# Kernel optimization log

Hardware: AMD Instinct MI355X
Metric: run time of the kernel (lower is better)

The kernel has to match this reference:

```python
import jax, jax.numpy as jnp
import numpy as np
from functools import partial

N, F_IN, P, OUT, E = 100000, 8, 12, 32, 3200000


def setup_inputs() -> dict:
    key = jax.random.key(0)
    ks = jax.random.split(key, 20)
    x = jax.random.normal(ks[0], (N, F_IN, P), dtype=jnp.float32)
    edge_index = jax.random.randint(ks[1], (2, E), 0, N, dtype=jnp.int64)
    edge_weight = jax.random.uniform(ks[2], (E,), dtype=jnp.float32)
    s = 1.0 / np.sqrt(F_IN)
    s2 = 1.0 / np.sqrt(2 * OUT)
    u = lambda k, sh, sc: jax.random.uniform(k, sh, jnp.float32, -sc, sc)
    params = dict(
        Wz=u(ks[3], (F_IN, OUT), s), bz=u(ks[4], (OUT,), s),
        Wr=u(ks[5], (F_IN, OUT), s), br=u(ks[6], (OUT,), s),
        Wh=u(ks[7], (F_IN, OUT), s), bh=u(ks[8], (OUT,), s),
        Lz=u(ks[9], (2 * OUT, OUT), s2), lbz=u(ks[10], (OUT,), s2),
        Lr=u(ks[11], (2 * OUT, OUT), s2), lbr=u(ks[12], (OUT,), s2),
        Lh=u(ks[13], (2 * OUT, OUT), s2), lbh=u(ks[14], (OUT,), s2),
        att=jax.random.uniform(ks[15], (P,), jnp.float32),
        Wp=u(ks[16], (OUT, 1), 1.0 / np.sqrt(OUT)), bp=u(ks[17], (1,), 1.0 / np.sqrt(OUT)),
    )
    return {"x": x, "edge_index": edge_index, "edge_weight": edge_weight, **params}


def reference(x, edge_index, edge_weight, Wz, bz, Wr, br, Wh, bh,
              Lz, lbz, Lr, lbr, Lh, lbh, att, Wp, bp):
    n = x.shape[0]
    # GCN normalization with self-loops: D^-1/2 (A + I) D^-1/2
    loop = jnp.arange(n)
    src = jnp.concatenate([edge_index[0], loop])
    dst = jnp.concatenate([edge_index[1], loop])
    w = jnp.concatenate([edge_weight, jnp.ones((n,), edge_weight.dtype)])
    deg = jax.ops.segment_sum(w, dst, num_segments=n)
    dinv = jnp.where(deg > 0, jax.lax.rsqrt(jnp.maximum(deg, 1e-30)), 0.0)
    norm = dinv[src] * w * dinv[dst]  # [E+N]

    def prop(X):  # gather-scale-scatter aggregation, X: [N, OUT]
        return jax.ops.segment_sum(X[src] * norm[:, None], dst, num_segments=n)

    def cell(H, Xt):  # TGCN GRU cell, Xt: [N, F_IN]
        cz = prop(Xt @ Wz) + bz
        cr = prop(Xt @ Wr) + br
        ch = prop(Xt @ Wh) + bh
        Z = jax.nn.sigmoid(jnp.concatenate([cz, H], axis=1) @ Lz + lbz)
        R = jax.nn.sigmoid(jnp.concatenate([cr, H], axis=1) @ Lr + lbr)
        Ht = jnp.tanh(jnp.concatenate([ch, R * H], axis=1) @ Lh + lbh)
        return Z * H + (1.0 - Z) * Ht

    probs = jax.nn.softmax(att)
    Xts = jnp.moveaxis(x, -1, 0)  # [P, N, F_IN]

    def scan_fn(carry, inp):
        H, acc = carry
        Xt, p = inp
        Hn = cell(H, Xt)
        return (Hn, acc + p * Hn), None

    H0 = jnp.zeros((n, OUT), x.dtype)
    (_, Hacc), _ = jax.lax.scan(scan_fn, (H0, H0), (Xts, probs))

    h = jax.nn.relu(Hacc)  # dropout is identity in eval mode
    delta = h @ Wp + bp  # [N, 1]
    out = jax.nn.relu(delta + x[:, 1, -1:])
    return out
```

## Files before the change

### kernel.cpp

```cpp
#include <hip/hip_runtime.h>
#include <cstddef>

typedef __attribute__((ext_vector_type(8))) short bf16x8;
typedef __attribute__((ext_vector_type(4))) float f32x4;

#define MFMA_B16(a, b, c) __builtin_amdgcn_mfma_f32_16x16x32_bf16(a, b, c, 0, 0, 0)

#define DEV_INLINE __device__ __forceinline__

#define NPB 128
#define NPB_SHIFT 7
#define NOCT 8
#define OCT_SHIFT 14

#define QSCALE (127.0f / 6.0f)
#define QDEC   (6.0f / 127.0f)

DEV_INLINE float rcp_fast(float x) { return __builtin_amdgcn_rcpf(x); }
DEV_INLINE float sigf(float x) { return rcp_fast(1.0f + __expf(-x)); }
DEV_INLINE float tanh_fast(float x) { return 1.0f - 2.0f * rcp_fast(__expf(2.0f * x) + 1.0f); }

DEV_INLINE unsigned short f2bf(float f) {
    union { float f; unsigned u; } v; v.f = f;
    unsigned r = v.u + 0x7fffu + ((v.u >> 16) & 1u);
    return (unsigned short)(r >> 16);
}

DEV_INLINE unsigned cvt_pk_bf16(float lo, float hi) {
    unsigned r;
    asm("v_cvt_pk_bf16_f32 %0, %1, %2" : "=v"(r) : "v"(lo), "v"(hi));
    return r;
}
DEV_INLINE float bf2f(unsigned short h) {
    union { unsigned u; float f; } t; t.u = ((unsigned)h) << 16; return t.f;
}

__global__ __launch_bounds__(256) void k_cast(const float* __restrict__ x,
                                              signed char* __restrict__ Xb8, int n) {
    __shared__ float s[64 * 97];
    const int tid = threadIdx.x;
    const int nbase = blockIdx.x * 64;
    const int lim = n * 96;
    const int base_elem = nbase * 96;

#pragma unroll
    for (int j = 0; j < 6; j++) {
        int g = j * 1024 + tid * 4;
        int gg = base_elem + g;
        if (gg + 4 <= lim) {
            float4 v = *(const float4*)(x + gg);
            int node = g / 96;
            int e = g - node * 96;
            float* p = &s[node * 97 + e];
            p[0] = v.x; p[1] = v.y; p[2] = v.z; p[3] = v.w;
        }
    }
    __syncthreads();

    const int nloc = tid >> 2;
    const int c = tid & 3;
    const int node = nbase + nloc;
    if (node < n) {
        const float* row = &s[nloc * 97];
        signed char* orow = Xb8 + (size_t)node * 96;
#pragma unroll
        for (int q = 0; q < 3; q++) {
            int t = c + 4 * q;
            unsigned w0 = 0u, w1 = 0u;
#pragma unroll
            for (int f = 0; f < 4; f++) {
                int qv = __float2int_rn(row[f * 12 + t] * QSCALE);
                qv = max(-127, min(127, qv));
                w0 |= ((unsigned)qv & 0xFFu) << (8 * f);
            }
#pragma unroll
            for (int f = 4; f < 8; f++) {
                int qv = __float2int_rn(row[f * 12 + t] * QSCALE);
                qv = max(-127, min(127, qv));
                w1 |= ((unsigned)qv & 0xFFu) << (8 * (f - 4));
            }
            uint2 vv = {w0, w1};
            *(uint2*)(orow + c * 8 + 32 * q) = vv;
        }
    }
}

__global__ __launch_bounds__(1024) void k_p3(const int* __restrict__ ei,
                                             const float* __restrict__ ew,
                                             unsigned* __restrict__ bucketCursor,
                                             unsigned* __restrict__ EB, int E) {
    __shared__ unsigned hist[1024];
    __shared__ unsigned bbase[1024];
    const int t = threadIdx.x;
    hist[t] = 0u;
    __syncthreads();
    const int base = blockIdx.x * 8192 + t * 8;
    unsigned key[8]; unsigned rk[8]; int bkt[8];
#pragma unroll
    for (int q = 0; q < 8; q++) {
        int e = base + q;
        if (e < E) {
            int d = ei[(size_t)E + e];
            int s = ei[e];
            unsigned w8 = min(255u, (unsigned)(ew[e] * 256.0f));
            bkt[q] = d >> NPB_SHIFT;
            key[q] = (unsigned)s | ((unsigned)(d & (NPB - 1)) << 17) | (w8 << 24);
            rk[q] = atomicAdd(&hist[bkt[q]], 1u);
        } else bkt[q] = -1;
    }
    __syncthreads();
    if (hist[t]) bbase[t] = atomicAdd(bucketCursor + t, hist[t]);
    __syncthreads();
#pragma unroll
    for (int q = 0; q < 8; q++) {
        if (bkt[q] >= 0) EB[(size_t)bbase[bkt[q]] + rk[q]] = key[q];
    }
}

__global__ __launch_bounds__(1024) void k_p2(const unsigned* __restrict__ bucketCursor,
                                             unsigned* __restrict__ bucketCnt,
                                             unsigned* __restrict__ bucketBase,
                                             int* __restrict__ rowptr,
                                             int NB, int N, int E, int CAP) {
    __shared__ unsigned ts[1024];
    const int t = threadIdx.x;
    unsigned v = (t < NB) ? (bucketCursor[t] - (unsigned)(t * CAP)) : 0u;
    ts[t] = v;
    __syncthreads();
    for (int off = 1; off < 1024; off <<= 1) {
        unsigned a = ts[t];
        unsigned b = (t >= off) ? ts[t - off] : 0u;
        __syncthreads();
        ts[t] = a + b;
        __syncthreads();
    }
    if (t < NB) {
        bucketBase[t] = ts[t] - v;
        bucketCnt[t] = v;
    }
    if (t == 0) rowptr[N] = E;
}

__global__ __launch_bounds__(1024) void k_p4(const unsigned* __restrict__ EB,
                                             const unsigned* __restrict__ bucketBase,
                                             const unsigned* __restrict__ bucketCnt,
                                             int* __restrict__ rowptr,
                                             float* __restrict__ dinv,
                                             unsigned* __restrict__ ckey,
                                             unsigned short* __restrict__ ccoef,
                                             int N, int CAP) {
    __shared__ unsigned cnt[NPB * NOCT];
    __shared__ unsigned lrow[NPB * NOCT];
    __shared__ float degs[NPB];
    __shared__ float sdinv[NPB];
    const int t = threadIdx.x;
    const int b = blockIdx.x;
    const size_t sbase = (size_t)b * CAP;
    const unsigned bbase = bucketBase[b];
    const unsigned bcnt = bucketCnt[b];
    cnt[t] = 0u;
    if (t < NPB) degs[t] = 0.0f;
    __syncthreads();

    unsigned key[8]; unsigned rk[8];
#pragma unroll
    for (int q = 0; q < 8; q++) {
        unsigned i = (unsigned)t + (unsigned)q * 1024u;
        if (i < bcnt) {
            unsigned it = EB[sbase + i];
            key[q] = it;
            unsigned dl = (it >> 17) & (NPB - 1);
            unsigned oct = (it & 0x1FFFFu) >> OCT_SHIFT;
            float w = ((float)(it >> 24) + 0.5f) * (1.0f / 256.0f);
            rk[q] = atomicAdd(&cnt[dl * NOCT + oct], 1u);
            atomicAdd(&degs[dl], w);
        }
    }
    __syncthreads();

    unsigned own = cnt[t];
    lrow[t] = own;
    __syncthreads();
    for (int off = 1; off < NPB * NOCT; off <<= 1) {
        unsigned a = lrow[t];
        unsigned c = (t >= off) ? lrow[t - off] : 0u;
        __syncthreads();
        lrow[t] = a + c;
        __syncthreads();
    }
    lrow[t] = lrow[t] - own;
    __syncthreads();
    if (t < NPB) {
        float dv = rsqrtf(degs[t] + 1.0f);
        sdinv[t] = dv;
        int node = b * NPB + t;
        if (node < N) { rowptr[node] = (int)(bbase + lrow[t * NOCT]); dinv[node] = dv; }
    }
    __syncthreads();

#pragma unroll
    for (int q = 0; q < 8; q++) {
        unsigned i = (unsigned)t + (unsigned)q * 1024u;
        if (i < bcnt) {
            unsigned it = key[q];
            unsigned dl = (it >> 17) & (NPB - 1);
            unsigned src = it & 0x1FFFFu;
            unsigned oct = src >> OCT_SHIFT;
            float w = ((float)(it >> 24) + 0.5f) * (1.0f / 256.0f);
            unsigned pos = bbase + lrow[dl * NOCT + oct] + rk[q];
            ckey[pos] = src;
            ccoef[pos] = f2bf(w * sdinv[dl] * QDEC);
        }
    }
}

__global__ __launch_bounds__(256) void k_wprep(const float* __restrict__ Wz, const float* __restrict__ Wr,
                                               const float* __restrict__ Wh,
                                               const float* __restrict__ Lz, const float* __restrict__ Lr,
                                               const float* __restrict__ Lh,
                                               const float* __restrict__ bz, const float* __restrict__ br,
                                               const float* __restrict__ bh,
                                               const float* __restrict__ lbz, const float* __restrict__ lbr,
                                               const float* __restrict__ lbh,
                                               float* __restrict__ WC,
                                               unsigned* __restrict__ bucketCursor, int NB, int CAP) {
    int tid = threadIdx.x;
    for (int b = tid; b < NB; b += 256) bucketCursor[b] = (unsigned)(b * CAP);
    for (int e = tid; e < 2048; e += 256) {
        int j = e >> 5, k = e & 31;
        const float* L = (j < 32) ? Lz : Lr;
        WC[e] = L[(32 + k) * 32 + (j & 31)];
    }
    for (int e = tid; e < 512; e += 256) {
        int j = e >> 3, f = e & 7;
        const float* L = (j < 32) ? Lz : Lr;
        const float* W = (j < 32) ? Wz : Wr;
        int jj = j & 31;
        float s = 0.0f;
        for (int i = 0; i < 32; i++) s += W[f * 32 + i] * L[i * 32 + jj];
        WC[2048 + e] = s;
    }
    for (int e = tid; e < 1024; e += 256) {
        int j = e >> 5, k = e & 31;
        WC[2560 + e] = Lh[(32 + k) * 32 + j];
    }
    for (int e = tid; e < 256; e += 256) {
        int j = e >> 3, f = e & 7;
        float s = 0.0f;
        for (int i = 0; i < 32; i++) s += Wh[f * 32 + i] * Lh[i * 32 + j];
        WC[3584 + e] = s;
    }
    if (tid < 64) {
        int j = tid;
        const float* L = (j < 32) ? Lz : Lr;
        const float* b = (j < 32) ? bz : br;
        const float* lb = (j < 32) ? lbz : lbr;
        int jj = j & 31;
        float s = lb[jj];
        for (int i = 0; i < 32; i++) s += b[i] * L[i * 32 + jj];
        WC[3840 + j] = s;
    }
    if (tid < 32) {
        float s = lbh[tid];
        for (int i = 0; i < 32; i++) s += bh[i] * Lh[i * 32 + tid];
        WC[3904 + tid] = s;
    }
}

__global__ __launch_bounds__(256) void k_pullgru(const signed char* __restrict__ Xb8,
                                                 const float* __restrict__ dinv,
                                                 const int* __restrict__ rowptr,
                                                 const unsigned* __restrict__ ckey,
                                                 const unsigned short* __restrict__ ccoef,
                                                 const float* __restrict__ x,
                                                 const float* __restrict__ WC,
                                                 const float* __restrict__ att,
                                                 const float* __restrict__ Wp,
                                                 const float* __restrict__ bp,
                                                 float* __restrict__ out, int n) {
    __shared__ __align__(16) unsigned short sH[4][16 * 40];
    __shared__ __align__(16) unsigned short sRH[4][16 * 40];
    __shared__ __align__(16) unsigned short sXp[4][12 * 16 * 8];
    __shared__ __align__(16) unsigned short zblk[4][8];

    const int tid = threadIdx.x;
    const int wv = tid >> 6;
    const int l = tid & 63;

    unsigned short* SH = sH[wv];
    unsigned short* SRH = sRH[wv];
    unsigned short* SXP = sXp[wv];

    {
        const int ln = tid >> 2;
        const int c = tid & 3;
        const int nl = ln & 15;
        const int d = min(blockIdx.x * 64 + ln, n - 1);

        float di = dinv[d];
        float sl = di * di * QDEC;
        float a[24];
        {
            const signed char* xr = Xb8 + (size_t)d * 96 + c * 8;
#pragma unroll
            for (int q = 0; q < 3; q++) {
                uint2 v = *(const uint2*)(xr + 32 * q);
                a[q * 8 + 0] = sl * (float)(signed char)(v.x);
                a[q * 8 + 1] = sl * (float)(signed char)(v.x >> 8);
                a[q * 8 + 2] = sl * (float)(signed char)(v.x >> 16);
                a[q * 8 + 3] = sl * (float)(signed char)(v.x >> 24);
                a[q * 8 + 4] = sl * (float)(signed char)(v.y);
                a[q * 8 + 5] = sl * (float)(signed char)(v.y >> 8);
                a[q * 8 + 6] = sl * (float)(signed char)(v.y >> 16);
                a[q * 8 + 7] = sl * (float)(signed char)(v.y >> 24);
            }
        }
        int lo = rowptr[d], hi = rowptr[d + 1];
        int e = lo;

#define ACC8(vv, cf, q)                                                     \
    do {                                                                    \
        a[(q) * 8 + 0] += (cf) * (float)(signed char)((vv).x);              \
        a[(q) * 8 + 1] += (cf) * (float)(signed char)((vv).x >> 8);         \
        a[(q) * 8 + 2] += (cf) * (float)(signed char)((vv).x >> 16);        \
        a[(q) * 8 + 3] += (cf) * (float)(signed char)((vv).x >> 24);        \
        a[(q) * 8 + 4] += (cf) * (float)(signed char)((vv).y);              \
        a[(q) * 8 + 5] += (cf) * (float)(signed char)((vv).y >> 8);         \
        a[(q) * 8 + 6] += (cf) * (float)(signed char)((vv).y >> 16);        \
        a[(q) * 8 + 7] += (cf) * (float)(signed char)((vv).y >> 24);        \
    } while (0)

        for (; e + 4 <= hi; e += 4) {
            unsigned k0 = ckey[e + 0];
            unsigned k1 = ckey[e + 1];
            unsigned k2 = ckey[e + 2];
            unsigned k3 = ckey[e + 3];
            float ds0 = dinv[k0];
            float ds1 = dinv[k1];
            float ds2 = dinv[k2];
            float ds3 = dinv[k3];
            const signed char* x0 = Xb8 + (size_t)k0 * 96 + c * 8;
            const signed char* x1 = Xb8 + (size_t)k1 * 96 + c * 8;
            const signed char* x2 = Xb8 + (size_t)k2 * 96 + c * 8;
            const signed char* x3 = Xb8 + (size_t)k3 * 96 + c * 8;
            uint2 v0[3], v1[3], v2[3], v3[3];
#pragma unroll
            for (int q = 0; q < 3; q++) v0[q] = *(const uint2*)(x0 + 32 * q);
#pragma unroll
            for (int q = 0; q < 3; q++) v1[q] = *(const uint2*)(x1 + 32 * q);
#pragma unroll
            for (int q = 0; q < 3; q++) v2[q] = *(const uint2*)(x2 + 32 * q);
#pragma unroll
            for (int q = 0; q < 3; q++) v3[q] = *(const uint2*)(x3 + 32 * q);
            float c0 = bf2f(ccoef[e + 0]) * ds0;
            float c1 = bf2f(ccoef[e + 1]) * ds1;
            float c2 = bf2f(ccoef[e + 2]) * ds2;
            float c3 = bf2f(ccoef[e + 3]) * ds3;
#pragma unroll
            for (int q = 0; q < 3; q++) ACC8(v0[q], c0, q);
#pragma unroll
            for (int q = 0; q < 3; q++) ACC8(v1[q], c1, q);
#pragma unroll
            for (int q = 0; q < 3; q++) ACC8(v2[q], c2, q);
#pragma unroll
            for (int q = 0; q < 3; q++) ACC8(v3[q], c3, q);
        }
        for (; e < hi; e++) {
            unsigned k = ckey[e];
            float cf = bf2f(ccoef[e]) * dinv[k];
            const signed char* xs = Xb8 + (size_t)k * 96 + c * 8;
            uint2 vv[3];
#pragma unroll
            for (int q = 0; q < 3; q++) vv[q] = *(const uint2*)(xs + 32 * q);
#pragma unroll
            for (int q = 0; q < 3; q++) ACC8(vv[q], cf, q);
        }
#undef ACC8

#pragma unroll
        for (int q = 0; q < 3; q++) {
            int t = c + 4 * q;
            unsigned w0 = cvt_pk_bf16(a[q * 8 + 0], a[q * 8 + 1]);
            unsigned w1 = cvt_pk_bf16(a[q * 8 + 2], a[q * 8 + 3]);
            unsigned w2 = cvt_pk_bf16(a[q * 8 + 4], a[q * 8 + 5]);
            unsigned w3 = cvt_pk_bf16(a[q * 8 + 6], a[q * 8 + 7]);
            uint4 vv = {w0, w1, w2, w3};
            *(uint4*)(&SXP[t * 128 + nl * 8]) = vv;
        }
    }

    const int lo16 = l & 15;
    const int g = l >> 4;
    const int base = blockIdx.x * 64 + wv * 16;

    for (int i = l; i < 16 * 40 / 2; i += 64) ((unsigned*)SH)[i] = 0u;
    if (l < 4) ((unsigned*)zblk[wv])[l] = 0u;

    const float* WZRH_H = WC;
    const float* WZR_X = WC + 2048;
    const float* WH_H = WC + 2560;
    const float* WH_X = WC + 3584;
    const float* BZR = WC + 3840;
    const float* BH = WC + 3904;

    bf16x8 wZRH[4], wZRX[4], wHH[2], wHX[2];
#pragma unroll
    for (int mt = 0; mt < 4; mt++) {
        int j = mt * 16 + lo16;
#pragma unroll
        for (int e = 0; e < 8; e++) {
            wZRH[mt][e] = (short)f2bf(WZRH_H[j * 32 + g * 8 + e]);
            wZRX[mt][e] = (g == 0) ? (short)f2bf(WZR_X[j * 8 + e]) : (short)0;
        }
    }
#pragma unroll
    for (int mt = 0; mt < 2; mt++) {
        int j = mt * 16 + lo16;
#pragma unroll
        for (int e = 0; e < 8; e++) {
            wHH[mt][e] = (short)f2bf(WH_H[j * 32 + g * 8 + e]);
            wHX[mt][e] = (g == 0) ? (short)f2bf(WH_X[j * 8 + e]) : (short)0;
        }
    }

    float bzr[4][4], bhh[2][4], wpr[2][4];
#pragma unroll
    for (int mt = 0; mt < 4; mt++)
#pragma unroll
        for (int r = 0; r < 4; r++) bzr[mt][r] = BZR[mt * 16 + 4 * g + r];
#pragma unroll
    for (int mt = 0; mt < 2; mt++)
#pragma unroll
        for (int r = 0; r < 4; r++) {
            bhh[mt][r] = BH[mt * 16 + 4 * g + r];
            wpr[mt][r] = Wp[mt * 16 + 4 * g + r];
        }

    float am = att[0];
    for (int t = 1; t < 12; t++) am = fmaxf(am, att[t]);
    float ad = 0.0f;
    for (int t = 0; t < 12; t++) ad += __expf(att[t] - am);
    float inv_ad = rcp_fast(ad);

    float H[2][4], acc[2][4];
#pragma unroll
    for (int mt = 0; mt < 2; mt++)
#pragma unroll
        for (int r = 0; r < 4; r++) { H[mt][r] = 0.0f; acc[mt][r] = 0.0f; }

    const f32x4 kc = {0.0f, 0.0f, 0.0f, 0.0f};

#pragma unroll 1
    for (int t = 0; t < 12; t++) {
        float pt = __expf(att[t] - am) * inv_ad;

        bf16x8 bH = *(const bf16x8*)(&SH[lo16 * 40 + g * 8]);
        const unsigned short* px = (g == 0) ? &SXP[t * 128 + lo16 * 8] : &zblk[wv][0];
        bf16x8 bX = *(const bf16x8*)px;

        float Z[2][4];
#pragma unroll
        for (int mt = 0; mt < 2; mt++) {
            f32x4 d = MFMA_B16(wZRH[mt], bH, kc);
            d = MFMA_B16(wZRX[mt], bX, d);
#pragma unroll
            for (int r = 0; r < 4; r++) Z[mt][r] = sigf(d[r] + bzr[mt][r]);
        }

#pragma unroll
        for (int mt = 2; mt < 4; mt++) {
            f32x4 d = MFMA_B16(wZRH[mt], bH, kc);
            d = MFMA_B16(wZRX[mt], bX, d);
            float rh[4];
#pragma unroll
            for (int r = 0; r < 4; r++)
                rh[r] = H[mt - 2][r] * sigf(d[r] + bzr[mt][r]);
            uint2 w;
            w.x = cvt_pk_bf16(rh[0], rh[1]);
            w.y = cvt_pk_bf16(rh[2], rh[3]);
            *(uint2*)(&SRH[lo16 * 40 + (mt - 2) * 16 + 4 * g]) = w;
        }

        bf16x8 bR = *(const bf16x8*)(&SRH[lo16 * 40 + g * 8]);

#pragma unroll
        for (int mt = 0; mt < 2; mt++) {
            f32x4 d = MFMA_B16(wHH[mt], bR, kc);
            d = MFMA_B16(wHX[mt], bX, d);
#pragma unroll
            for (int r = 0; r < 4; r++) {
                float T = tanh_fast(d[r] + bhh[mt][r]);
                float z = Z[mt][r];
                float h = T + z * (H[mt][r] - T);
                H[mt][r] = h;
                acc[mt][r] += pt * h;
            }
            uint2 w;
            w.x = cvt_pk_bf16(H[mt][0], H[mt][1]);
            w.y = cvt_pk_bf16(H[mt][2], H[mt][3]);
            *(uint2*)(&SH[lo16 * 40 + mt * 16 + 4 * g]) = w;
        }
    }

    float p = 0.0f;
#pragma unroll
    for (int mt = 0; mt < 2; mt++)
#pragma unroll
        for (int r = 0; r < 4; r++) p += fmaxf(acc[mt][r], 0.0f) * wpr[mt][r];
    p += __shfl_xor(p, 16);
    p += __shfl_xor(p, 32);
    if (l < 16) {
        int nd = base + l;
        if (nd < n) out[nd] = fmaxf(p + bp[0] + x[(size_t)nd * 96 + 23], 0.0f);
    }
}

static inline size_t align_up(size_t v, size_t a) { return (v + a - 1) & ~(a - 1); }

extern "C" void kernel_launch(void* const* d_in, const int* in_sizes, int n_in,
                              void* d_out, int out_size, void* d_ws, size_t ws_size,
                              hipStream_t stream) {
    const float* x   = (const float*)d_in[0];
    const int*   ei  = (const int*)d_in[1];
    const float* ew  = (const float*)d_in[2];
    const float* Wz  = (const float*)d_in[3];
    const float* bz  = (const float*)d_in[4];
    const float* Wr  = (const float*)d_in[5];
    const float* br  = (const float*)d_in[6];
    const float* Wh  = (const float*)d_in[7];
    const float* bh  = (const float*)d_in[8];
    const float* Lz  = (const float*)d_in[9];
    const float* lbz = (const float*)d_in[10];
    const float* Lr  = (const float*)d_in[11];
    const float* lbr = (const float*)d_in[12];
    const float* Lh  = (const float*)d_in[13];
    const float* lbh = (const float*)d_in[14];
    const float* att = (const float*)d_in[15];
    const float* Wp  = (const float*)d_in[16];
    const float* bp  = (const float*)d_in[17];
    float* out = (float*)d_out;

    const int N = in_sizes[0] / 96;
    const int E = in_sizes[2];
    const int NB = (N + NPB - 1) / NPB;
    const int CAP = 6144;

    char* ws = (char*)d_ws;
    size_t off = 0;
    float* dinv   = (float*)(ws + off); off = align_up(off + (size_t)N * 4, 256);
    int*   rowptr = (int*)  (ws + off); off = align_up(off + (size_t)(N + 1) * 4, 256);
    unsigned* bucketCnt    = (unsigned*)(ws + off); off = align_up(off + 1024 * 4, 256);
    unsigned* bucketBase   = (unsigned*)(ws + off); off = align_up(off + 1024 * 4, 256);
    unsigned* bucketCursor = (unsigned*)(ws + off); off = align_up(off + 1024 * 4, 256);
    unsigned* ckey  = (unsigned*)(ws + off); off = align_up(off + (size_t)E * 4, 256);
    unsigned short* ccoef = (unsigned short*)(ws + off); off = align_up(off + (size_t)E * 2, 256);
    signed char* Xb8 = (signed char*)(ws + off); off = align_up(off + (size_t)N * 96, 256);
    unsigned* EB = (unsigned*)(ws + off); off = align_up(off + (size_t)NB * CAP * 4, 256);
    float* WC = (float*)(ws + off); off = align_up(off + 3936 * 4, 256);

    int eb8 = (E + 8191) / 8192;

    k_wprep<<<1, 256, 0, stream>>>(Wz, Wr, Wh, Lz, Lr, Lh, bz, br, bh, lbz, lbr, lbh,
                                   WC, bucketCursor, NB, CAP);
    k_cast<<<(N + 63) / 64, 256, 0, stream>>>(x, Xb8, N);
    k_p3<<<eb8, 1024, 0, stream>>>(ei, ew, bucketCursor, EB, E);
    k_p2<<<1, 1024, 0, stream>>>(bucketCursor, bucketCnt, bucketBase, rowptr, NB, N, E, CAP);
    k_p4<<<NB, 1024, 0, stream>>>(EB, bucketBase, bucketCnt, rowptr, dinv, ckey, ccoef, N, CAP);
    k_pullgru<<<(N + 63) / 64, 256, 0, stream>>>(Xb8, dinv, rowptr, ckey, ccoef,
                                                 x, WC, att, Wp, bp, out, N);
}
```

Baseline: 267.9 us.

## Split fused pull+GRU kernel and prefold source dinv into edge coefficients

Splits the fused gather-aggregate plus GRU kernel into a standalone pull kernel that writes bf16 aggregated features to a global buffer, and a GRU kernel that reads them back into shared memory. A new pass multiplies each edge coefficient by the source node's dinv ahead of time, removing the random dinv gather from the pull loop. The intent is to free the pull phase from the GRU kernel's register and LDS pressure so occupancy improves. The cost is an extra N×96×2-byte round trip, an extra pass over all edges, two more launches, and an extra bf16 rounding of the coefficient.

```diff
diff --git a/kernel.cpp b/kernel.cpp
--- a/kernel.cpp
+++ b/kernel.cpp
@@ -214,6 +214,122 @@
     }
 }
 
+__global__ __launch_bounds__(256) void k_p5(unsigned short* __restrict__ ccoef,
+                                            const unsigned* __restrict__ ckey,
+                                            const float* __restrict__ dinv, int E) {
+    int i = (blockIdx.x * 256 + threadIdx.x) * 4;
+    if (i + 4 <= E) {
+        uint4 k = *(const uint4*)(ckey + i);
+        ushort4 cc = *(const ushort4*)(ccoef + i);
+        ushort4 o;
+        o.x = f2bf(bf2f(cc.x) * dinv[k.x]);
+        o.y = f2bf(bf2f(cc.y) * dinv[k.y]);
+        o.z = f2bf(bf2f(cc.z) * dinv[k.z]);
+        o.w = f2bf(bf2f(cc.w) * dinv[k.w]);
+        *(ushort4*)(ccoef + i) = o;
+    } else {
+        for (; i < E; i++) ccoef[i] = f2bf(bf2f(ccoef[i]) * dinv[ckey[i]]);
+    }
+}
+
+__global__ __launch_bounds__(256) void k_pull(const signed char* __restrict__ Xb8,
+                                              const float* __restrict__ dinv,
+                                              const int* __restrict__ rowptr,
+                                              const unsigned* __restrict__ ckey,
+                                              const unsigned short* __restrict__ ccoef,
+                                              unsigned short* __restrict__ Xp, int n) {
+    int gid = blockIdx.x * 256 + threadIdx.x;
+    int d = gid >> 2;
+    int c = gid & 3;
+    if (d >= n) return;
+    float di = dinv[d];
+    float sl = di * di * QDEC;
+    float a[24];
+    {
+        const signed char* xr = Xb8 + (size_t)d * 96 + c * 8;
+#pragma unroll
+        for (int q = 0; q < 3; q++) {
+            uint2 v = *(const uint2*)(xr + 32 * q);
+            a[q * 8 + 0] = sl * (float)(signed char)(v.x);
+            a[q * 8 + 1] = sl * (float)(signed char)(v.x >> 8);
+            a[q * 8 + 2] = sl * (float)(signed char)(v.x >> 16);
+            a[q * 8 + 3] = sl * (float)(signed char)(v.x >> 24);
+            a[q * 8 + 4] = sl * (float)(signed char)(v.y);
+            a[q * 8 + 5] = sl * (float)(signed char)(v.y >> 8);
+            a[q * 8 + 6] = sl * (float)(signed char)(v.y >> 16);
+            a[q * 8 + 7] = sl * (float)(signed char)(v.y >> 24);
+        }
+    }
+    int lo = rowptr[d], hi = rowptr[d + 1];
+    int e = lo;
+
+#define ACC8(vv, cf, q)                                                     \
+    do {                                                                    \
+        a[(q) * 8 + 0] += (cf) * (float)(signed char)((vv).x);              \
+        a[(q) * 8 + 1] += (cf) * (float)(signed char)((vv).x >> 8);         \
+        a[(q) * 8 + 2] += (cf) * (float)(signed char)((vv).x >> 16);        \
+        a[(q) * 8 + 3] += (cf) * (float)(signed char)((vv).x >> 24);        \
+        a[(q) * 8 + 4] += (cf) * (float)(signed char)((vv).y);              \
+        a[(q) * 8 + 5] += (cf) * (float)(signed char)((vv).y >> 8);         \
+        a[(q) * 8 + 6] += (cf) * (float)(signed char)((vv).y >> 16);        \
+        a[(q) * 8 + 7] += (cf) * (float)(signed char)((vv).y >> 24);        \
+    } while (0)
+
+    for (; e + 4 <= hi; e += 4) {
+        unsigned k0 = ckey[e + 0];
+        unsigned k1 = ckey[e + 1];
+        unsigned k2 = ckey[e + 2];
+        unsigned k3 = ckey[e + 3];
+        const signed char* x0 = Xb8 + (size_t)k0 * 96 + c * 8;
+        const signed char* x1 = Xb8 + (size_t)k1 * 96 + c * 8;
+        const signed char* x2 = Xb8 + (size_t)k2 * 96 + c * 8;
+        const signed char* x3 = Xb8 + (size_t)k3 * 96 + c * 8;
+        uint2 v0[3], v1[3], v2[3], v3[3];
+#pragma unroll
+        for (int q = 0; q < 3; q++) v0[q] = *(const uint2*)(x0 + 32 * q);
+#pragma unroll
+        for (int q = 0; q < 3; q++) v1[q] = *(const uint2*)(x1 + 32 * q);
+#pragma unroll
+        for (int q = 0; q < 3; q++) v2[q] = *(const uint2*)(x2 + 32 * q);
+#pragma unroll
+        for (int q = 0; q < 3; q++) v3[q] = *(const uint2*)(x3 + 32 * q);
+        float c0 = bf2f(ccoef[e + 0]);
+        float c1 = bf2f(ccoef[e + 1]);
+        float c2 = bf2f(ccoef[e + 2]);
+        float c3 = bf2f(ccoef[e + 3]);
+#pragma unroll
+        for (int q = 0; q < 3; q++) ACC8(v0[q], c0, q);
+#pragma unroll
+        for (int q = 0; q < 3; q++) ACC8(v1[q], c1, q);
+#pragma unroll
+        for (int q = 0; q < 3; q++) ACC8(v2[q], c2, q);
+#pragma unroll
+        for (int q = 0; q < 3; q++) ACC8(v3[q], c3, q);
+    }
+    for (; e < hi; e++) {
+        unsigned k = ckey[e];
+        float cf = bf2f(ccoef[e]);
+        const signed char* xs = Xb8 + (size_t)k * 96 + c * 8;
+        uint2 vv[3];
+#pragma unroll
+        for (int q = 0; q < 3; q++) vv[q] = *(const uint2*)(xs + 32 * q);
+#pragma unroll
+        for (int q = 0; q < 3; q++) ACC8(vv[q], cf, q);
+    }
+#undef ACC8
+
+    unsigned short* o = Xp + (size_t)d * 96 + c * 8;
+#pragma unroll
+    for (int q = 0; q < 3; q++) {
+        unsigned w0 = cvt_pk_bf16(a[q * 8 + 0], a[q * 8 + 1]);
+        unsigned w1 = cvt_pk_bf16(a[q * 8 + 2], a[q * 8 + 3]);
+        unsigned w2 = cvt_pk_bf16(a[q * 8 + 4], a[q * 8 + 5]);
+        unsigned w3 = cvt_pk_bf16(a[q * 8 + 6], a[q * 8 + 7]);
+        uint4 vv = {w0, w1, w2, w3};
+        *(uint4*)(o + 32 * q) = vv;
+    }
+}
+
 __global__ __launch_bounds__(256) void k_wprep(const float* __restrict__ Wz, const float* __restrict__ Wr,
                                                const float* __restrict__ Wh,
                                                const float* __restrict__ Lz, const float* __restrict__ Lr,
@@ -267,17 +383,13 @@
     }
 }
 
-__global__ __launch_bounds__(256) void k_pullgru(const signed char* __restrict__ Xb8,
-                                                 const float* __restrict__ dinv,
-                                                 const int* __restrict__ rowptr,
-                                                 const unsigned* __restrict__ ckey,
-                                                 const unsigned short* __restrict__ ccoef,
-                                                 const float* __restrict__ x,
-                                                 const float* __restrict__ WC,
-                                                 const float* __restrict__ att,
-                                                 const float* __restrict__ Wp,
-                                                 const float* __restrict__ bp,
-                                                 float* __restrict__ out, int n) {
+__global__ __launch_bounds__(256) void k_gru(const unsigned short* __restrict__ Xp,
+                                             const float* __restrict__ x,
+                                             const float* __restrict__ WC,
+                                             const float* __restrict__ att,
+                                             const float* __restrict__ Wp,
+                                             const float* __restrict__ bp,
+                                             float* __restrict__ out, int n) {
     __shared__ __align__(16) unsigned short sH[4][16 * 40];
     __shared__ __align__(16) unsigned short sRH[4][16 * 40];
     __shared__ __align__(16) unsigned short sXp[4][12 * 16 * 8];
@@ -286,115 +398,25 @@
     const int tid = threadIdx.x;
     const int wv = tid >> 6;
     const int l = tid & 63;
+    const int lo16 = l & 15;
+    const int g = l >> 4;
+    const int base = blockIdx.x * 64 + wv * 16;
 
     unsigned short* SH = sH[wv];
     unsigned short* SRH = sRH[wv];
     unsigned short* SXP = sXp[wv];
 
-    {
-        const int ln = tid >> 2;
-        const int c = tid & 3;
-        const int nl = ln & 15;
-        const int d = min(blockIdx.x * 64 + ln, n - 1);
-
-        float di = dinv[d];
-        float sl = di * di * QDEC;
-        float a[24];
-        {
-            const signed char* xr = Xb8 + (size_t)d * 96 + c * 8;
-#pragma unroll
-            for (int q = 0; q < 3; q++) {
-                uint2 v = *(const uint2*)(xr + 32 * q);
-                a[q * 8 + 0] = sl * (float)(signed char)(v.x);
-                a[q * 8 + 1] = sl * (float)(signed char)(v.x >> 8);
-                a[q * 8 + 2] = sl * (float)(signed char)(v.x >> 16);
-                a[q * 8 + 3] = sl * (float)(signed char)(v.x >> 24);
-                a[q * 8 + 4] = sl * (float)(signed char)(v.y);
-                a[q * 8 + 5] = sl * (float)(signed char)(v.y >> 8);
-                a[q * 8 + 6] = sl * (float)(signed char)(v.y >> 16);
-                a[q * 8 + 7] = sl * (float)(signed char)(v.y >> 24);
-            }
-        }
-        int lo = rowptr[d], hi = rowptr[d + 1];
-        int e = lo;
-
-#define ACC8(vv, cf, q)                                                     \
-    do {                                                                    \
-        a[(q) * 8 + 0] += (cf) * (float)(signed char)((vv).x);              \
-        a[(q) * 8 + 1] += (cf) * (float)(signed char)((vv).x >> 8);         \
-        a[(q) * 8 + 2] += (cf) * (float)(signed char)((vv).x >> 16);        \
-        a[(q) * 8 + 3] += (cf) * (float)(signed char)((vv).x >> 24);        \
-        a[(q) * 8 + 4] += (cf) * (float)(signed char)((vv).y);              \
-        a[(q) * 8 + 5] += (cf) * (float)(signed char)((vv).y >> 8);         \
-        a[(q) * 8 + 6] += (cf) * (float)(signed char)((vv).y >> 16);        \
-        a[(q) * 8 + 7] += (cf) * (float)(signed char)((vv).y >> 24);        \
-    } while (0)
-
-        for (; e + 4 <= hi; e += 4) {
-            unsigned k0 = ckey[e + 0];
-            unsigned k1 = ckey[e + 1];
-            unsigned k2 = ckey[e + 2];
-            unsigned k3 = ckey[e + 3];
-            float ds0 = dinv[k0];
-            float ds1 = dinv[k1];
-            float ds2 = dinv[k2];
-            float ds3 = dinv[k3];
-            const signed char* x0 = Xb8 + (size_t)k0 * 96 + c * 8;
-            const signed char* x1 = Xb8 + (size_t)k1 * 96 + c * 8;
-            const signed char* x2 = Xb8 + (size_t)k2 * 96 + c * 8;
-            const signed char* x3 = Xb8 + (size_t)k3 * 96 + c * 8;
-            uint2 v0[3], v1[3], v2[3], v3[3];
-#pragma unroll
-            for (int q = 0; q < 3; q++) v0[q] = *(const uint2*)(x0 + 32 * q);
-#pragma unroll
-            for (int q = 0; q < 3; q++) v1[q] = *(const uint2*)(x1 + 32 * q);
-#pragma unroll
-            for (int q = 0; q < 3; q++) v2[q] = *(const uint2*)(x2 + 32 * q);
-#pragma unroll
-            for (int q = 0; q < 3; q++) v3[q] = *(const uint2*)(x3 + 32 * q);
-            float c0 = bf2f(ccoef[e + 0]) * ds0;
-            float c1 = bf2f(ccoef[e + 1]) * ds1;
-            float c2 = bf2f(ccoef[e + 2]) * ds2;
-            float c3 = bf2f(ccoef[e + 3]) * ds3;
-#pragma unroll
-            for (int q = 0; q < 3; q++) ACC8(v0[q], c0, q);
-#pragma unroll
-            for (int q = 0; q < 3; q++) ACC8(v1[q], c1, q);
-#pragma unroll
-            for (int q = 0; q < 3; q++) ACC8(v2[q], c2, q);
-#pragma unroll
-            for (int q = 0; q < 3; q++) ACC8(v3[q], c3, q);
-        }
-        for (; e < hi; e++) {
-            unsigned k = ckey[e];
-            float cf = bf2f(ccoef[e]) * dinv[k];
-            const signed char* xs = Xb8 + (size_t)k * 96 + c * 8;
-            uint2 vv[3];
-#pragma unroll
-            for (int q = 0; q < 3; q++) vv[q] = *(const uint2*)(xs + 32 * q);
-#pragma unroll
-            for (int q = 0; q < 3; q++) ACC8(vv[q], cf, q);
-        }
-#undef ACC8
-
-#pragma unroll
-        for (int q = 0; q < 3; q++) {
-            int t = c + 4 * q;
-            unsigned w0 = cvt_pk_bf16(a[q * 8 + 0], a[q * 8 + 1]);
-            unsigned w1 = cvt_pk_bf16(a[q * 8 + 2], a[q * 8 + 3]);
-            unsigned w2 = cvt_pk_bf16(a[q * 8 + 4], a[q * 8 + 5]);
-            unsigned w3 = cvt_pk_bf16(a[q * 8 + 6], a[q * 8 + 7]);
-            uint4 vv = {w0, w1, w2, w3};
-            *(uint4*)(&SXP[t * 128 + nl * 8]) = vv;
-        }
-    }
-
-    const int lo16 = l & 15;
-    const int g = l >> 4;
-    const int base = blockIdx.x * 64 + wv * 16;
-
+#pragma unroll
+    for (int j = 0; j < 3; j++) {
+        int i = l + 64 * j;
+        int nd = min(base + (i & 15), n - 1);
+        int q = i >> 4;
+        uint4 v = *(const uint4*)(Xp + (size_t)nd * 96 + q * 8);
+        *(uint4*)(&SXP[q * 128 + (i & 15) * 8]) = v;
+    }
     for (int i = l; i < 16 * 40 / 2; i += 64) ((unsigned*)SH)[i] = 0u;
     if (l < 4) ((unsigned*)zblk[wv])[l] = 0u;
+    __syncthreads();
 
     const float* WZRH_H = WC;
     const float* WZR_X = WC + 2048;
@@ -555,6 +577,7 @@
     unsigned* ckey  = (unsigned*)(ws + off); off = align_up(off + (size_t)E * 4, 256);
     unsigned short* ccoef = (unsigned short*)(ws + off); off = align_up(off + (size_t)E * 2, 256);
     signed char* Xb8 = (signed char*)(ws + off); off = align_up(off + (size_t)N * 96, 256);
+    unsigned short* Xp = (unsigned short*)(ws + off); off = align_up(off + (size_t)N * 96 * 2, 256);
     unsigned* EB = (unsigned*)(ws + off); off = align_up(off + (size_t)NB * CAP * 4, 256);
     float* WC = (float*)(ws + off); off = align_up(off + 3936 * 4, 256);
 
@@ -566,6 +589,7 @@
     k_p3<<<eb8, 1024, 0, stream>>>(ei, ew, bucketCursor, EB, E);
     k_p2<<<1, 1024, 0, stream>>>(bucketCursor, bucketCnt, bucketBase, rowptr, NB, N, E, CAP);
     k_p4<<<NB, 1024, 0, stream>>>(EB, bucketBase, bucketCnt, rowptr, dinv, ckey, ccoef, N, CAP);
-    k_pullgru<<<(N + 63) / 64, 256, 0, stream>>>(Xb8, dinv, rowptr, ckey, ccoef,
-                                                 x, WC, att, Wp, bp, out, N);
-}
+    k_p5<<<(E / 4 + 255) / 256, 256, 0, stream>>>(ccoef, ckey, dinv, E);
+    k_pull<<<(N * 4 + 255) / 256, 256, 0, stream>>>(Xb8, dinv, rowptr, ckey, ccoef, Xp, N);
+    k_gru<<<(N + 63) / 64, 256, 0, stream>>>(Xp, x, WC, att, Wp, bp, out, N);
+}
```

After: 274.0 us. 2.3% more time.

## Split fused pull+GRU kernel into separate aggregation and GRU kernels

Applied to the files above, without the earlier changes.

Splits the fused gather/aggregate plus GRU kernel into two kernels. The aggregation kernel writes the propagated features as bf16 to a new global buffer, and the GRU kernel reads them straight from global memory instead of shared memory. The aim is to decouple the latency-bound gather from the MFMA-heavy GRU, so each runs with its own occupancy and without shared-memory staging. In exchange it adds a round trip of roughly N×96×2 bytes through global memory and one more kernel launch.

```diff
diff --git a/kernel.cpp b/kernel.cpp
--- a/kernel.cpp
+++ b/kernel.cpp
@@ -214,6 +214,108 @@
     }
 }
 
+__global__ __launch_bounds__(256) void k_pull(const signed char* __restrict__ Xb8,
+                                              const float* __restrict__ dinv,
+                                              const int* __restrict__ rowptr,
+                                              const unsigned* __restrict__ ckey,
+                                              const unsigned short* __restrict__ ccoef,
+                                              unsigned short* __restrict__ Xp, int n) {
+    int gid = blockIdx.x * 256 + threadIdx.x;
+    int d = gid >> 2;
+    int c = gid & 3;
+    if (d >= n) return;
+    float di = dinv[d];
+    float sl = di * di * QDEC;
+    float a[24];
+    {
+        const signed char* xr = Xb8 + (size_t)d * 96 + c * 8;
+#pragma unroll
+        for (int q = 0; q < 3; q++) {
+            uint2 v = *(const uint2*)(xr + 32 * q);
+            a[q * 8 + 0] = sl * (float)(signed char)(v.x);
+            a[q * 8 + 1] = sl * (float)(signed char)(v.x >> 8);
+            a[q * 8 + 2] = sl * (float)(signed char)(v.x >> 16);
+            a[q * 8 + 3] = sl * (float)(signed char)(v.x >> 24);
+            a[q * 8 + 4] = sl * (float)(signed char)(v.y);
+            a[q * 8 + 5] = sl * (float)(signed char)(v.y >> 8);
+            a[q * 8 + 6] = sl * (float)(signed char)(v.y >> 16);
+            a[q * 8 + 7] = sl * (float)(signed char)(v.y >> 24);
+        }
+    }
+    int lo = rowptr[d], hi = rowptr[d + 1];
+    int e = lo;
+
+#define ACC8(vv, cf, q)                                                     \
+    do {                                                                    \
+        a[(q) * 8 + 0] += (cf) * (float)(signed char)((vv).x);              \
+        a[(q) * 8 + 1] += (cf) * (float)(signed char)((vv).x >> 8);         \
+        a[(q) * 8 + 2] += (cf) * (float)(signed char)((vv).x >> 16);        \
+        a[(q) * 8 + 3] += (cf) * (float)(signed char)((vv).x >> 24);        \
+        a[(q) * 8 + 4] += (cf) * (float)(signed char)((vv).y);              \
+        a[(q) * 8 + 5] += (cf) * (float)(signed char)((vv).y >> 8);         \
+        a[(q) * 8 + 6] += (cf) * (float)(signed char)((vv).y >> 16);        \
+        a[(q) * 8 + 7] += (cf) * (float)(signed char)((vv).y >> 24);        \
+    } while (0)
+
+    for (; e + 4 <= hi; e += 4) {
+        unsigned k0 = ckey[e + 0];
+        unsigned k1 = ckey[e + 1];
+        unsigned k2 = ckey[e + 2];
+        unsigned k3 = ckey[e + 3];
+        float ds0 = dinv[k0];
+        float ds1 = dinv[k1];
+        float ds2 = dinv[k2];
+        float ds3 = dinv[k3];
+        const signed char* x0 = Xb8 + (size_t)k0 * 96 + c * 8;
+        const signed char* x1 = Xb8 + (size_t)k1 * 96 + c * 8;
+        const signed char* x2 = Xb8 + (size_t)k2 * 96 + c * 8;
+        const signed char* x3 = Xb8 + (size_t)k3 * 96 + c * 8;
+        uint2 v0[3], v1[3], v2[3], v3[3];
+#pragma unroll
+        for (int q = 0; q < 3; q++) v0[q] = *(const uint2*)(x0 + 32 * q);
+#pragma unroll
+        for (int q = 0; q < 3; q++) v1[q] = *(const uint2*)(x1 + 32 * q);
+#pragma unroll
+        for (int q = 0; q < 3; q++) v2[q] = *(const uint2*)(x2 + 32 * q);
+#pragma unroll
+        for (int q = 0; q < 3; q++) v3[q] = *(const uint2*)(x3 + 32 * q);
+        float c0 = bf2f(ccoef[e + 0]) * ds0;
+        float c1 = bf2f(ccoef[e + 1]) * ds1;
+        float c2 = bf2f(ccoef[e + 2]) * ds2;
+        float c3 = bf2f(ccoef[e + 3]) * ds3;
+#pragma unroll
+        for (int q = 0; q < 3; q++) ACC8(v0[q], c0, q);
+#pragma unroll
+        for (int q = 0; q < 3; q++) ACC8(v1[q], c1, q);
+#pragma unroll
+        for (int q = 0; q < 3; q++) ACC8(v2[q], c2, q);
+#pragma unroll
+        for (int q = 0; q < 3; q++) ACC8(v3[q], c3, q);
+    }
+    for (; e < hi; e++) {
+        unsigned k = ckey[e];
+        float cf = bf2f(ccoef[e]) * dinv[k];
+        const signed char* xs = Xb8 + (size_t)k * 96 + c * 8;
+        uint2 vv[3];
+#pragma unroll
+        for (int q = 0; q < 3; q++) vv[q] = *(const uint2*)(xs + 32 * q);
+#pragma unroll
+        for (int q = 0; q < 3; q++) ACC8(vv[q], cf, q);
+    }
+#undef ACC8
+
+    unsigned short* o = Xp + (size_t)d * 96 + c * 8;
+#pragma unroll
+    for (int q = 0; q < 3; q++) {
+        unsigned w0 = cvt_pk_bf16(a[q * 8 + 0], a[q * 8 + 1]);
+        unsigned w1 = cvt_pk_bf16(a[q * 8 + 2], a[q * 8 + 3]);
+        unsigned w2 = cvt_pk_bf16(a[q * 8 + 4], a[q * 8 + 5]);
+        unsigned w3 = cvt_pk_bf16(a[q * 8 + 6], a[q * 8 + 7]);
+        uint4 vv = {w0, w1, w2, w3};
+        *(uint4*)(o + 32 * q) = vv;
+    }
+}
+
 __global__ __launch_bounds__(256) void k_wprep(const float* __restrict__ Wz, const float* __restrict__ Wr,
                                                const float* __restrict__ Wh,
                                                const float* __restrict__ Lz, const float* __restrict__ Lr,
@@ -267,134 +369,29 @@
     }
 }
 
-__global__ __launch_bounds__(256) void k_pullgru(const signed char* __restrict__ Xb8,
-                                                 const float* __restrict__ dinv,
-                                                 const int* __restrict__ rowptr,
-                                                 const unsigned* __restrict__ ckey,
-                                                 const unsigned short* __restrict__ ccoef,
-                                                 const float* __restrict__ x,
-                                                 const float* __restrict__ WC,
-                                                 const float* __restrict__ att,
-                                                 const float* __restrict__ Wp,
-                                                 const float* __restrict__ bp,
-                                                 float* __restrict__ out, int n) {
+__global__ __launch_bounds__(256) void k_gru(const unsigned short* __restrict__ Xp,
+                                             const float* __restrict__ x,
+                                             const float* __restrict__ WC,
+                                             const float* __restrict__ att,
+                                             const float* __restrict__ Wp,
+                                             const float* __restrict__ bp,
+                                             float* __restrict__ out, int n) {
     __shared__ __align__(16) unsigned short sH[4][16 * 40];
     __shared__ __align__(16) unsigned short sRH[4][16 * 40];
-    __shared__ __align__(16) unsigned short sXp[4][12 * 16 * 8];
-    __shared__ __align__(16) unsigned short zblk[4][8];
 
     const int tid = threadIdx.x;
     const int wv = tid >> 6;
     const int l = tid & 63;
-
-    unsigned short* SH = sH[wv];
-    unsigned short* SRH = sRH[wv];
-    unsigned short* SXP = sXp[wv];
-
-    {
-        const int ln = tid >> 2;
-        const int c = tid & 3;
-        const int nl = ln & 15;
-        const int d = min(blockIdx.x * 64 + ln, n - 1);
-
-        float di = dinv[d];
-        float sl = di * di * QDEC;
-        float a[24];
-        {
-            const signed char* xr = Xb8 + (size_t)d * 96 + c * 8;
-#pragma unroll
-            for (int q = 0; q < 3; q++) {
-                uint2 v = *(const uint2*)(xr + 32 * q);
-                a[q * 8 + 0] = sl * (float)(signed char)(v.x);
-                a[q * 8 + 1] = sl * (float)(signed char)(v.x >> 8);
-                a[q * 8 + 2] = sl * (float)(signed char)(v.x >> 16);
-                a[q * 8 + 3] = sl * (float)(signed char)(v.x >> 24);
-                a[q * 8 + 4] = sl * (float)(signed char)(v.y);
-                a[q * 8 + 5] = sl * (float)(signed char)(v.y >> 8);
-                a[q * 8 + 6] = sl * (float)(signed char)(v.y >> 16);
-                a[q * 8 + 7] = sl * (float)(signed char)(v.y >> 24);
-            }
-        }
-        int lo = rowptr[d], hi = rowptr[d + 1];
-        int e = lo;
-
-#define ACC8(vv, cf, q)                                                     \
-    do {                                                                    \
-        a[(q) * 8 + 0] += (cf) * (float)(signed char)((vv).x);              \
-        a[(q) * 8 + 1] += (cf) * (float)(signed char)((vv).x >> 8);         \
-        a[(q) * 8 + 2] += (cf) * (float)(signed char)((vv).x >> 16);        \
-        a[(q) * 8 + 3] += (cf) * (float)(signed char)((vv).x >> 24);        \
-        a[(q) * 8 + 4] += (cf) * (float)(signed char)((vv).y);              \
-        a[(q) * 8 + 5] += (cf) * (float)(signed char)((vv).y >> 8);         \
-        a[(q) * 8 + 6] += (cf) * (float)(signed char)((vv).y >> 16);        \
-        a[(q) * 8 + 7] += (cf) * (float)(signed char)((vv).y >> 24);        \
-    } while (0)
-
-        for (; e + 4 <= hi; e += 4) {
-            unsigned k0 = ckey[e + 0];
-            unsigned k1 = ckey[e + 1];
-            unsigned k2 = ckey[e + 2];
-            unsigned k3 = ckey[e + 3];
-            float ds0 = dinv[k0];
-            float ds1 = dinv[k1];
-            float ds2 = dinv[k2];
-            float ds3 = dinv[k3];
-            const signed char* x0 = Xb8 + (size_t)k0 * 96 + c * 8;
-            const signed char* x1 = Xb8 + (size_t)k1 * 96 + c * 8;
-            const signed char* x2 = Xb8 + (size_t)k2 * 96 + c * 8;
-            const signed char* x3 = Xb8 + (size_t)k3 * 96 + c * 8;
-            uint2 v0[3], v1[3], v2[3], v3[3];
-#pragma unroll
-            for (int q = 0; q < 3; q++) v0[q] = *(const uint2*)(x0 + 32 * q);
-#pragma unroll
-            for (int q = 0; q < 3; q++) v1[q] = *(const uint2*)(x1 + 32 * q);
-#pragma unroll
-            for (int q = 0; q < 3; q++) v2[q] = *(const uint2*)(x2 + 32 * q);
-#pragma unroll
-            for (int q = 0; q < 3; q++) v3[q] = *(const uint2*)(x3 + 32 * q);
-            float c0 = bf2f(ccoef[e + 0]) * ds0;
-            float c1 = bf2f(ccoef[e + 1]) * ds1;
-            float c2 = bf2f(ccoef[e + 2]) * ds2;
-            float c3 = bf2f(ccoef[e + 3]) * ds3;
-#pragma unroll
-            for (int q = 0; q < 3; q++) ACC8(v0[q], c0, q);
-#pragma unroll
-            for (int q = 0; q < 3; q++) ACC8(v1[q], c1, q);
-#pragma unroll
-            for (int q = 0; q < 3; q++) ACC8(v2[q], c2, q);
-#pragma unroll
-            for (int q = 0; q < 3; q++) ACC8(v3[q], c3, q);
-        }
-        for (; e < hi; e++) {
-            unsigned k = ckey[e];
-            float cf = bf2f(ccoef[e]) * dinv[k];
-            const signed char* xs = Xb8 + (size_t)k * 96 + c * 8;
-            uint2 vv[3];
-#pragma unroll
-            for (int q = 0; q < 3; q++) vv[q] = *(const uint2*)(xs + 32 * q);
-#pragma unroll
-            for (int q = 0; q < 3; q++) ACC8(vv[q], cf, q);
-        }
-#undef ACC8
-
-#pragma unroll
-        for (int q = 0; q < 3; q++) {
-            int t = c + 4 * q;
-            unsigned w0 = cvt_pk_bf16(a[q * 8 + 0], a[q * 8 + 1]);
-            unsigned w1 = cvt_pk_bf16(a[q * 8 + 2], a[q * 8 + 3]);
-            unsigned w2 = cvt_pk_bf16(a[q * 8 + 4], a[q * 8 + 5]);
-            unsigned w3 = cvt_pk_bf16(a[q * 8 + 6], a[q * 8 + 7]);
-            uint4 vv = {w0, w1, w2, w3};
-            *(uint4*)(&SXP[t * 128 + nl * 8]) = vv;
-        }
-    }
-
     const int lo16 = l & 15;
     const int g = l >> 4;
     const int base = blockIdx.x * 64 + wv * 16;
 
+    unsigned short* SH = sH[wv];
+    unsigned short* SRH = sRH[wv];
+
     for (int i = l; i < 16 * 40 / 2; i += 64) ((unsigned*)SH)[i] = 0u;
-    if (l < 4) ((unsigned*)zblk[wv])[l] = 0u;
+
+    const unsigned short* xrow = Xp + (size_t)min(base + lo16, n - 1) * 96;
 
     const float* WZRH_H = WC;
     const float* WZR_X = WC + 2048;
@@ -449,14 +446,16 @@
         for (int r = 0; r < 4; r++) { H[mt][r] = 0.0f; acc[mt][r] = 0.0f; }
 
     const f32x4 kc = {0.0f, 0.0f, 0.0f, 0.0f};
+    const bf16x8 bz8 = {0, 0, 0, 0, 0, 0, 0, 0};
 
 #pragma unroll 1
     for (int t = 0; t < 12; t++) {
         float pt = __expf(att[t] - am) * inv_ad;
 
+        bf16x8 xv = *(const bf16x8*)(xrow + t * 8);
+        bf16x8 bX = (g == 0) ? xv : bz8;
+
         bf16x8 bH = *(const bf16x8*)(&SH[lo16 * 40 + g * 8]);
-        const unsigned short* px = (g == 0) ? &SXP[t * 128 + lo16 * 8] : &zblk[wv][0];
-        bf16x8 bX = *(const bf16x8*)px;
 
         float Z[2][4];
 #pragma unroll
@@ -555,6 +554,7 @@
     unsigned* ckey  = (unsigned*)(ws + off); off = align_up(off + (size_t)E * 4, 256);
     unsigned short* ccoef = (unsigned short*)(ws + off); off = align_up(off + (size_t)E * 2, 256);
     signed char* Xb8 = (signed char*)(ws + off); off = align_up(off + (size_t)N * 96, 256);
+    unsigned short* Xp = (unsigned short*)(ws + off); off = align_up(off + (size_t)N * 96 * 2, 256);
     unsigned* EB = (unsigned*)(ws + off); off = align_up(off + (size_t)NB * CAP * 4, 256);
     float* WC = (float*)(ws + off); off = align_up(off + 3936 * 4, 256);
 
@@ -566,6 +566,6 @@
     k_p3<<<eb8, 1024, 0, stream>>>(ei, ew, bucketCursor, EB, E);
     k_p2<<<1, 1024, 0, stream>>>(bucketCursor, bucketCnt, bucketBase, rowptr, NB, N, E, CAP);
     k_p4<<<NB, 1024, 0, stream>>>(EB, bucketBase, bucketCnt, rowptr, dinv, ckey, ccoef, N, CAP);
-    k_pullgru<<<(N + 63) / 64, 256, 0, stream>>>(Xb8, dinv, rowptr, ckey, ccoef,
-                                                 x, WC, att, Wp, bp, out, N);
-}
+    k_pull<<<(N * 4 + 255) / 256, 256, 0, stream>>>(Xb8, dinv, rowptr, ckey, ccoef, Xp, N);
+    k_gru<<<(N + 63) / 64, 256, 0, stream>>>(Xp, x, WC, att, Wp, bp, out, N);
+}
```

Measured after the change: 277.0 us. 3.4% more time.
